# Kernel tuning notes

Hardware: AMD Instinct MI355X
Metric: run time of the kernel (lower is better)

## Reference

```python
import jax, jax.numpy as jnp
import numpy as np

EPS = 1e-5
B, N, NPOINT, K = 16, 4096, 1024, 32
IN_CH, OUT_CH = 64, 64


def index_points(points, idx):
    # points: [B, N, C], idx: [B, ...] -> [B, ..., C]
    b = points.shape[0]
    flat = idx.reshape(b, -1)
    out = jnp.take_along_axis(points, flat[:, :, None], axis=1)
    return out.reshape(idx.shape + (points.shape[-1],))


def bn2d(x, gamma, beta):
    # x: [B, C, H, W], batch-stat BN (training mode), biased variance
    m = x.mean(axis=(0, 2, 3), keepdims=True)
    v = x.var(axis=(0, 2, 3), keepdims=True)
    return gamma[None, :, None, None] * (x - m) / jnp.sqrt(v + EPS) + beta[None, :, None, None]


def bn1d(x, gamma, beta):
    # x: [B, C, L]
    m = x.mean(axis=(0, 2), keepdims=True)
    v = x.var(axis=(0, 2), keepdims=True)
    return gamma[None, :, None] * (x - m) / jnp.sqrt(v + EPS) + beta[None, :, None]


def conv1x1(x, w, b):
    # x: [B, C, H, W], w: [O, C], b: [O]
    return jnp.einsum('bchw,oc->bohw', x, w) + b[None, :, None, None]


def setup_inputs() -> dict:
    key = jax.random.key(0)
    ks = jax.random.split(key, 16)
    inp = {
        'xyz': jax.random.normal(ks[0], (B, N, 3), jnp.float32),
        'points': jax.random.normal(ks[1], (B, N, 61), jnp.float32),
        'local_coordinates': jax.random.normal(ks[2], (B, NPOINT * K, 3), jnp.float32),
        'neighbor_lists': jax.random.randint(ks[3], (B, NPOINT, K), 0, N),
        'data_idx': jax.random.randint(ks[4], (B, NPOINT), 0, N),
        # WeightNet: 3 -> 16 -> 16 -> OUT_CH, each conv1x1 + BN2d + relu
        'w0': jax.random.normal(ks[5], (16, 3), jnp.float32) * 0.1,
        'b0': jnp.zeros((16,), jnp.float32),
        'g0': jnp.ones((16,), jnp.float32),
        'be0': jnp.zeros((16,), jnp.float32),
        'w1': jax.random.normal(ks[6], (16, 16), jnp.float32) * 0.1,
        'b1': jnp.zeros((16,), jnp.float32),
        'g1': jnp.ones((16,), jnp.float32),
        'be1': jnp.zeros((16,), jnp.float32),
        'w2': jax.random.normal(ks[7], (OUT_CH, 16), jnp.float32) * 0.1,
        'b2': jnp.zeros((OUT_CH,), jnp.float32),
        'g2': jnp.ones((OUT_CH,), jnp.float32),
        'be2': jnp.zeros((OUT_CH,), jnp.float32),
        # bn_conv over IN_CH*OUT_CH channels
        'gc': jnp.ones((IN_CH * OUT_CH,), jnp.float32),
        'bc': jnp.zeros((IN_CH * OUT_CH,), jnp.float32),
        # linear IN_CH*OUT_CH -> OUT_CH
        'lw': jax.random.normal(ks[8], (IN_CH * OUT_CH, OUT_CH), jnp.float32) * 0.01,
        'lb': jnp.zeros((OUT_CH,), jnp.float32),
        # bn_linear
        'gl': jnp.ones((OUT_CH,), jnp.float32),
        'bl': jnp.zeros((OUT_CH,), jnp.float32),
    }
    return inp


def reference(xyz, points, local_coordinates, neighbor_lists, data_idx,
              w0, b0, g0, be0, w1, b1, g1, be1, w2, b2, g2, be2,
              gc, bc, lw, lb, gl, bl):
    new_xyz = index_points(xyz, data_idx)                       # [B, NPOINT, 3]
    pts = jnp.concatenate([points, xyz], axis=2)                # [B, N, IN_CH]
    grouped = index_points(pts, neighbor_lists)                 # [B, NPOINT, K, IN_CH]
    grouped = grouped.transpose(0, 1, 3, 2)                     # [B, NPOINT, IN_CH, K]

    # WeightNet on local coordinates
    lc = local_coordinates.reshape(B, NPOINT, K, 3).transpose(0, 3, 2, 1)  # [B, 3, K, NPOINT]
    h = jax.nn.relu(bn2d(conv1x1(lc, w0, b0), g0, be0))
    h = jax.nn.relu(bn2d(conv1x1(h, w1, b1), g1, be1))
    h = jax.nn.relu(bn2d(conv1x1(h, w2, b2), g2, be2))          # [B, OUT_CH, K, NPOINT]
    weights = h.transpose(0, 3, 2, 1)                            # [B, NPOINT, K, OUT_CH]

    # aggregate over neighbors: [B, NPOINT, IN_CH, OUT_CH]
    new_points = jnp.einsum('bnik,bnko->bnio', grouped, weights)
    new_points = new_points.reshape(B, NPOINT, IN_CH * OUT_CH)

    new_points = jax.nn.relu(
        bn1d(new_points.transpose(0, 2, 1), gc, bc).transpose(0, 2, 1))
    new_points = new_points @ lw + lb                            # [B, NPOINT, OUT_CH]
    new_points = bn1d(new_points.transpose(0, 2, 1), gl, bl).transpose(0, 2, 1)
    new_points = jax.nn.relu(new_points)
    return (new_xyz, new_points)
```

## Files before the change

kernel.cpp:

```cpp
#include <hip/hip_runtime.h>
#include <hip/hip_bf16.h>

#define BB 16
#define NN 4096
#define NPOINTS 1024
#define KK 32
#define NPTS (BB*NPOINTS)
#define NWN  (BB*NPOINTS*KK)
#define EPSF 1e-5f
#define SGBLK 512
#define SGIT  4

typedef unsigned short u16;
typedef u16  u16x8 __attribute__((ext_vector_type(8)));
typedef u16  u16x4 __attribute__((ext_vector_type(4)));
typedef short s16x8 __attribute__((ext_vector_type(8)));
typedef float f32x4 __attribute__((ext_vector_type(4)));
typedef float f32x4u __attribute__((ext_vector_type(4), aligned(4)));

__device__ __forceinline__ float bf(u16 u){
  union { unsigned int i; float f; } v; v.i = ((unsigned int)u) << 16; return v.f;
}
__device__ __forceinline__ u16 f2b(float f){
  __hip_bfloat16 h = __float2bfloat16(f);
  union { __hip_bfloat16 hh; u16 u; } v; v.hh = h; return v.u;
}


__global__ __launch_bounds__(256) void k_init(const float* xyz, const int* didx, float* out,
                                              const float* lw, u16* lwbt,
                                              const float* points, u16* ptsw,
                                              const float* lc, float* PA){
  int t = threadIdx.x;
  if (blockIdx.x < 64){
    int p = blockIdx.x * 256 + t;
    int b = p >> 10;
    int idx = didx[p];
    const float* src = xyz + ((size_t)(b * NN + idx)) * 3;
    float* dst = out + (size_t)p * 3;
    dst[0] = src[0]; dst[1] = src[1]; dst[2] = src[2];
  } else if (blockIdx.x < 128){
    __shared__ float T[64][65];
    int ib = blockIdx.x - 64;
    int kb = ib * 64;
    {
      int k = t >> 2, c4 = t & 3;
      #pragma unroll
      for (int j = 0; j < 4; ++j)
        *(f32x4*)&T[k][c4*16 + j*4] = *(const f32x4*)(lw + (size_t)(kb + k)*64 + c4*16 + j*4);
    }
    __syncthreads();
    {
      int n = t >> 2, k4 = t & 3;
      #pragma unroll
      for (int j = 0; j < 16; ++j){
        int k = k4*16 + j;
        lwbt[(size_t)n*4096 + k*64 + ib] = f2b(T[k][n]);
      }
    }
  } else if (blockIdx.x < 640){
    int gid0 = (blockIdx.x - 128) * 256 + t;
    #pragma unroll
    for (int rep = 0; rep < 4; ++rep){
      int idx = gid0 + rep * 131072;
      int row = idx >> 3, c8 = idx & 7;
      const float* prow = points + (size_t)row * 61;
      u16x8 g;
      if (c8 < 7){
        f32x4 lo = *(const f32x4u*)(prow + c8*8);
        f32x4 hi = *(const f32x4u*)(prow + c8*8 + 4);
        g[0]=f2b(lo.x); g[1]=f2b(lo.y); g[2]=f2b(lo.z); g[3]=f2b(lo.w);
        g[4]=f2b(hi.x); g[5]=f2b(hi.y); g[6]=f2b(hi.z); g[7]=f2b(hi.w);
      } else {
        const float* xr = xyz + (size_t)row * 3;
        f32x4 lo = *(const f32x4u*)(prow + 56);
        g[0]=f2b(lo.x); g[1]=f2b(lo.y); g[2]=f2b(lo.z); g[3]=f2b(lo.w);
        g[4]=f2b(prow[60]);
        g[5]=f2b(xr[0]); g[6]=f2b(xr[1]); g[7]=f2b(xr[2]);
      }
      *(u16x8*)(ptsw + (size_t)row*64 + c8*8) = g;
    }
  } else {
    int bid = blockIdx.x - 640;
    float a[9];
    #pragma unroll
    for (int r = 0; r < 9; ++r) a[r] = 0.f;
    size_t base = (size_t)bid * 1024 + t;
    for (int ip = 0; ip < 4; ++ip){
      size_t p = base + (size_t)ip * 256;
      float x0 = lc[p*3], x1 = lc[p*3+1], x2 = lc[p*3+2];
      a[0]+=x0; a[1]+=x1; a[2]+=x2;
      a[3]+=x0*x0; a[4]+=x0*x1; a[5]+=x0*x2;
      a[6]+=x1*x1; a[7]+=x1*x2; a[8]+=x2*x2;
    }
    #pragma unroll
    for (int m = 1; m < 64; m <<= 1){
      #pragma unroll
      for (int r = 0; r < 9; ++r) a[r] += __shfl_xor(a[r], m);
    }
    if ((t & 63) == 0){
      float* dst = PA + (size_t)(bid*4 + (t>>6)) * 16;
      f32x4 v0 = {a[0],a[1],a[2],a[3]}, v1 = {a[4],a[5],a[6],a[7]}, v2 = {a[8],0.f,0.f,0.f};
      *(f32x4*)dst = v0; *(f32x4*)(dst+4) = v1; *(f32x4*)(dst+8) = v2;
    }
  }
}

__global__ __launch_bounds__(256) void k_red0(const float* PA, const float* w0, const float* b0,
                                              const float* g0, const float* be0, float* F){
  __shared__ float ms[12];
  __shared__ float a0sh[16];
  int t = threadIdx.x;
  if (t < 12){
    float s0=0,s1=0,s2=0,s3=0;
    const float* p = PA + t;
    for (int r = 0; r < 2048; r += 4){
      s0 += p[(size_t)(r+0)*16]; s1 += p[(size_t)(r+1)*16];
      s2 += p[(size_t)(r+2)*16]; s3 += p[(size_t)(r+3)*16];
    }
    ms[t] = (s0+s1)+(s2+s3);
  }
  __syncthreads();
  if (t < 16){
    float wx = w0[t*3], wy = w0[t*3+1], wz = w0[t*3+2], bb = b0[t];
    float lin = wx*ms[0] + wy*ms[1] + wz*ms[2];
    float quad = wx*wx*ms[3] + wy*wy*ms[6] + wz*wz*ms[8]
               + 2.f*(wx*wy*ms[4] + wx*wz*ms[5] + wy*wz*ms[7]);
    float S = lin + (float)NWN * bb;
    float Q = quad + 2.f*bb*lin + (float)NWN*bb*bb;
    float m = S * (1.f/NWN);
    float v = Q * (1.f/NWN) - m*m;
    float a = g0[t] * rsqrtf(v + EPSF);
    float d = be0[t] - m*a;
    a0sh[t] = a;
    F[48+t] = a*bb + d;
  }
  __syncthreads();
  if (t < 48) F[t] = a0sh[t/3] * w0[t];
}

__global__ __launch_bounds__(256) void k_statG1(const float* lc, const float* F, float* PB){
  __shared__ f32x4 w0p[16];
  __shared__ __align__(16) u16 Ht[4][16*72];
  __shared__ float GS[4][16][17];
  __shared__ float SHs[4][16];
  int t = threadIdx.x;
  int w = t >> 6, l = t & 63;
  if (t < 16){
    f32x4 wv = {F[t*3], F[t*3+1], F[t*3+2], F[48+t]};
    w0p[t] = wv;
  }
  __syncthreads();
  f32x4 acc = {0.f,0.f,0.f,0.f};
  float sh[16];
  #pragma unroll
  for (int r = 0; r < 16; ++r) sh[r] = 0.f;
  u16* Hw = &Ht[w][0];
  for (int it = 0; it < SGIT; ++it){
    size_t p = (size_t)blockIdx.x * (SGIT*256) + (size_t)it*256 + w*64 + l;
    float x0 = lc[p*3], x1 = lc[p*3+1], x2 = lc[p*3+2];
    float h[16];
    #pragma unroll
    for (int oc = 0; oc < 16; ++oc){
      f32x4 wv = w0p[oc];
      h[oc] = fmaxf(0.f, wv.x*x0 + wv.y*x1 + wv.z*x2 + wv.w);
      sh[oc] += h[oc];
    }
    #pragma unroll
    for (int c = 0; c < 16; ++c) Hw[c*72 + l] = f2b(h[c]);
    __syncthreads();
    #pragma unroll
    for (int tt = 0; tt < 2; ++tt){
      s16x8 af = *(const s16x8*)&Hw[(l & 15)*72 + tt*32 + (l >> 4)*8];
      acc = __builtin_amdgcn_mfma_f32_16x16x32_bf16(af, af, acc, 0, 0, 0);
    }
    __syncthreads();
  }
  #pragma unroll
  for (int r = 0; r < 4; ++r)
    GS[w][(l>>4)*4 + r][l & 15] = acc[r];
  #pragma unroll
  for (int m = 1; m < 64; m <<= 1){
    #pragma unroll
    for (int r = 0; r < 16; ++r) sh[r] += __shfl_xor(sh[r], m);
  }
  if (l == 0){
    #pragma unroll
    for (int r = 0; r < 16; ++r) SHs[w][r] = sh[r];
  }
  __syncthreads();
  {
    int i = t >> 4, j = t & 15;
    float g = GS[0][i][j] + GS[1][i][j] + GS[2][i][j] + GS[3][i][j];
    PB[(size_t)blockIdx.x*272 + t] = g;
    if (t < 16)
      PB[(size_t)blockIdx.x*272 + 256 + t] = SHs[0][t]+SHs[1][t]+SHs[2][t]+SHs[3][t];
  }
}

__global__ __launch_bounds__(256) void k_statG2(const float* lc, const float* F,
                                                const u16* w1Bg, float* PB){
  __shared__ f32x4 w0p[16];
  __shared__ __align__(16) u16 Ht0[4][64*40];
  __shared__ __align__(16) u16 Ht1[4][16*72];
  __shared__ float GS[4][16][17];
  __shared__ float SHs[4][16];
  int t = threadIdx.x;
  int w = t >> 6, l = t & 63;
  if (t < 16){
    f32x4 wv = {F[t*3], F[t*3+1], F[t*3+2], F[48+t]};
    w0p[t] = wv;
  }
  s16x8 w1B = *(const s16x8*)&w1Bg[l*8];
  float b1f = F[320 + (l & 15)];
  u16* H0w = &Ht0[w][0];
  u16* H1w = &Ht1[w][0];
  {
    u16x8 z8 = {0,0,0,0,0,0,0,0};
    *(u16x8*)&H0w[l*40 + 16] = z8;
    *(u16x8*)&H0w[l*40 + 24] = z8;
  }
  __syncthreads();
  f32x4 acc = {0.f,0.f,0.f,0.f};
  float shloc = 0.f;
  for (int it = 0; it < SGIT; ++it){
    size_t p = (size_t)blockIdx.x * (SGIT*256) + (size_t)it*256 + w*64 + l;
    float x0 = lc[p*3], x1 = lc[p*3+1], x2 = lc[p*3+2];
    u16x8 p0, p1;
    #pragma unroll
    for (int oc = 0; oc < 8; ++oc){
      f32x4 wv = w0p[oc];
      p0[oc] = f2b(fmaxf(0.f, wv.x*x0 + wv.y*x1 + wv.z*x2 + wv.w));
    }
    #pragma unroll
    for (int oc = 0; oc < 8; ++oc){
      f32x4 wv = w0p[8+oc];
      p1[oc] = f2b(fmaxf(0.f, wv.x*x0 + wv.y*x1 + wv.z*x2 + wv.w));
    }
    *(u16x8*)&H0w[l*40]     = p0;
    *(u16x8*)&H0w[l*40 + 8] = p1;
    __syncthreads();
    #pragma unroll
    for (int mt = 0; mt < 4; ++mt){
      s16x8 af = *(const s16x8*)&H0w[(mt*16 + (l & 15))*40 + (l >> 4)*8];
      f32x4 c = {b1f, b1f, b1f, b1f};
      c = __builtin_amdgcn_mfma_f32_16x16x32_bf16(af, w1B, c, 0, 0, 0);
      #pragma unroll
      for (int r = 0; r < 4; ++r){
        float v = fmaxf(0.f, c[r]);
        shloc += v;
        H1w[(l & 15)*72 + mt*16 + (l >> 4)*4 + r] = f2b(v);
      }
    }
    __syncthreads();
    #pragma unroll
    for (int tt = 0; tt < 2; ++tt){
      s16x8 afg = *(const s16x8*)&H1w[(l & 15)*72 + tt*32 + (l >> 4)*8];
      acc = __builtin_amdgcn_mfma_f32_16x16x32_bf16(afg, afg, acc, 0, 0, 0);
    }
    __syncthreads();
  }
  #pragma unroll
  for (int r = 0; r < 4; ++r)
    GS[w][(l>>4)*4 + r][l & 15] = acc[r];
  shloc += __shfl_xor(shloc, 16);
  shloc += __shfl_xor(shloc, 32);
  if (l < 16) SHs[w][l] = shloc;
  __syncthreads();
  {
    int i = t >> 4, j = t & 15;
    float g = GS[0][i][j] + GS[1][i][j] + GS[2][i][j] + GS[3][i][j];
    PB[(size_t)blockIdx.x*272 + t] = g;
    if (t < 16)
      PB[(size_t)blockIdx.x*272 + 256 + t] = SHs[0][t]+SHs[1][t]+SHs[2][t]+SHs[3][t];
  }
}

__global__ __launch_bounds__(256) void k_red1(const float* PB, const float* w1, const float* b1,
                                              const float* g1, const float* be1, float* F,
                                              u16* w1Bg){
  __shared__ float red[272];
  __shared__ float a1sh[16];
  int t = threadIdx.x;
  for (int e = t; e < 272; e += 256){
    float s = 0.f;
    for (int r = 0; r < SGBLK; ++r) s += PB[(size_t)r*272 + e];
    red[e] = s;
  }
  __syncthreads();
  if (t < 16){
    float wv[16];
    #pragma unroll
    for (int ic = 0; ic < 16; ++ic) wv[ic] = w1[t*16+ic];
    float lin = 0.f;
    #pragma unroll
    for (int ic = 0; ic < 16; ++ic) lin += wv[ic]*red[256+ic];
    float quad = 0.f;
    for (int i = 0; i < 16; ++i){
      float ri = 0.f;
      #pragma unroll
      for (int j = 0; j < 16; ++j) ri += wv[j]*red[i*16+j];
      quad += wv[i]*ri;
    }
    float bb = b1[t];
    float S = lin + (float)NWN * bb;
    float Q = quad + 2.f*bb*lin + (float)NWN*bb*bb;
    float m = S * (1.f/NWN);
    float v = Q * (1.f/NWN) - m*m;
    float a = g1[t] * rsqrtf(v + EPSF);
    float d = be1[t] - m*a;
    a1sh[t] = a;
    F[320+t] = a*bb + d;
  }
  __syncthreads();
  F[64 + t] = a1sh[t >> 4] * w1[t];
  if (t < 64){
    int oc = t & 15, icb = (t >> 4) * 8;
    u16x8 fr;
    #pragma unroll
    for (int j = 0; j < 8; ++j){
      int ic = icb + j;
      fr[j] = (ic < 16) ? f2b(a1sh[oc] * w1[oc*16 + ic]) : (u16)0;
    }
    *(u16x8*)&w1Bg[t*8] = fr;
  }
}

__global__ __launch_bounds__(256) void k_red2(const float* PB, const float* w2, const float* b2,
                                              const float* g2, const float* be2, float* F,
                                              u16* w2Bg){
  __shared__ float red[272];
  __shared__ float a2sh[64];
  int t = threadIdx.x;
  for (int e = t; e < 272; e += 256){
    float s = 0.f;
    for (int r = 0; r < SGBLK; ++r) s += PB[(size_t)r*272 + e];
    red[e] = s;
  }
  __syncthreads();
  if (t < 64){
    float wv[16];
    #pragma unroll
    for (int ic = 0; ic < 16; ++ic) wv[ic] = w2[t*16+ic];
    float lin = 0.f;
    #pragma unroll
    for (int ic = 0; ic < 16; ++ic) lin += wv[ic]*red[256+ic];
    float quad = 0.f;
    for (int i = 0; i < 16; ++i){
      float ri = 0.f;
      #pragma unroll
      for (int j = 0; j < 16; ++j) ri += wv[j]*red[i*16+j];
      quad += wv[i]*ri;
    }
    float bb = b2[t];
    float S = lin + (float)NWN * bb;
    float Q = quad + 2.f*bb*lin + (float)NWN*bb*bb;
    float m = S * (1.f/NWN);
    float v = Q * (1.f/NWN) - m*m;
    float a = g2[t] * rsqrtf(v + EPSF);
    float d = be2[t] - m*a;
    a2sh[t] = a;
    F[1360+t] = a*bb + d;
  }
  __syncthreads();
  for (int i = t; i < 1024; i += 256) F[336+i] = a2sh[i >> 4] * w2[i];
  {
    int ot = t >> 6, lane = t & 63;
    int oc = ot*16 + (lane & 15), icb = ((lane >> 4)) * 8;
    u16x8 fr;
    #pragma unroll
    for (int j = 0; j < 8; ++j){
      int ic = icb + j;
      fr[j] = (ic < 16) ? f2b(a2sh[oc] * w2[oc*16 + ic]) : (u16)0;
    }
    *(u16x8*)&w2Bg[t*8] = fr;
  }
}

__global__ __launch_bounds__(256) void k_main(const float* lcg, const int* nbrg,
    const u16* ptsw, const float* F,
    const u16* w1Bg, const u16* w2Bg,
    u16* npw){
  __shared__ __align__(16) u16 Gr[2][64*40];
  __shared__ __align__(16) u16 WrBuf[2][64*40];
  __shared__ __align__(16) u16 H1bf[2][32*40];
  int t = threadIdx.x;
  int w = t >> 6, l = t & 63;
  int p0 = blockIdx.x * 2;
  s16x8 w1B  = *(const s16x8*)&w1Bg[l*8];
  s16x8 w2B0 = *(const s16x8*)&w2Bg[(0*64 + l)*8];
  s16x8 w2B1 = *(const s16x8*)&w2Bg[(1*64 + l)*8];
  s16x8 w2B2 = *(const s16x8*)&w2Bg[(2*64 + l)*8];
  s16x8 w2B3 = *(const s16x8*)&w2Bg[(3*64 + l)*8];
  float b1f  = F[320 + (l & 15)];
  float b2f0 = F[1360 +  0 + (l & 15)];
  float b2f1 = F[1360 + 16 + (l & 15)];
  float b2f2 = F[1360 + 32 + (l & 15)];
  float b2f3 = F[1360 + 48 + (l & 15)];
  int oc0 = (t & 7) * 2;
  f32x4 w0a = {F[oc0*3], F[oc0*3+1], F[oc0*3+2], F[48+oc0]};
  f32x4 w0b = {F[oc0*3+3], F[oc0*3+4], F[oc0*3+5], F[48+oc0+1]};
  {
    int k = t >> 3, c = 16 + (t & 7)*2;
    *(unsigned int*)&WrBuf[0][k*40 + c] = 0u;
    *(unsigned int*)&WrBuf[1][k*40 + c] = 0u;
    *(unsigned int*)&H1bf[0][k*40 + c] = 0u;
    *(unsigned int*)&H1bf[1][k*40 + c] = 0u;
  }
  {
    int kg = w*8 + (l >> 3), c8 = l & 7;
    int kphys = ((w ^ (c8 & 3)) << 3) + (l >> 3);
    #pragma unroll
    for (int pt = 0; pt < 2; ++pt){
      int point = p0 + pt;
      int bbp = point >> 10;
      int n = nbrg[(size_t)point*32 + kg];
      u16x8 g = *(const u16x8*)(ptsw + (size_t)(bbp * NN + n)*64 + c8*8);
      #pragma unroll
      for (int j = 0; j < 8; ++j)
        Gr[pt][(c8*8 + j)*40 + kphys] = g[j];
    }
  }
  {
    int k = t >> 3;
    #pragma unroll
    for (int pt = 0; pt < 2; ++pt){
      const float* xp = lcg + (size_t)(p0 + pt)*96 + k*3;
      float x0 = xp[0], x1 = xp[1], x2 = xp[2];
      WrBuf[pt][k*40 + oc0]     = f2b(fmaxf(0.f, w0a.x*x0 + w0a.y*x1 + w0a.z*x2 + w0a.w));
      WrBuf[pt][k*40 + oc0 + 1] = f2b(fmaxf(0.f, w0b.x*x0 + w0b.y*x1 + w0b.z*x2 + w0b.w));
    }
  }
  __syncthreads();
  {
    int pt = w >> 1, kt = w & 1;
    s16x8 af = *(const s16x8*)&WrBuf[pt][(kt*16 + (l & 15))*40 + (l >> 4)*8];
    f32x4 acc = {b1f, b1f, b1f, b1f};
    acc = __builtin_amdgcn_mfma_f32_16x16x32_bf16(af, w1B, acc, 0, 0, 0);
    #pragma unroll
    for (int r = 0; r < 4; ++r)
      H1bf[pt][(kt*16 + (l >> 4)*4 + r)*40 + (l & 15)] = f2b(fmaxf(0.f, acc[r]));
  }
  __syncthreads();
  {
    int pt = w & 1, kt = w >> 1;
    s16x8 af = *(const s16x8*)&H1bf[pt][(kt*16 + (l & 15))*40 + (l >> 4)*8];
    int kbase = kt*16 + (l >> 4)*4;
    f32x4 a0c = {b2f0,b2f0,b2f0,b2f0};
    a0c = __builtin_amdgcn_mfma_f32_16x16x32_bf16(af, w2B0, a0c, 0, 0, 0);
    u16x4 s0v; s0v[0]=f2b(fmaxf(0.f,a0c[0])); s0v[1]=f2b(fmaxf(0.f,a0c[1]));
    s0v[2]=f2b(fmaxf(0.f,a0c[2])); s0v[3]=f2b(fmaxf(0.f,a0c[3]));
    *(u16x4*)&WrBuf[pt][( 0 + (l & 15))*40 + kbase] = s0v;
    f32x4 a1c = {b2f1,b2f1,b2f1,b2f1};
    a1c = __builtin_amdgcn_mfma_f32_16x16x32_bf16(af, w2B1, a1c, 0, 0, 0);
    u16x4 s1v; s1v[0]=f2b(fmaxf(0.f,a1c[0])); s1v[1]=f2b(fmaxf(0.f,a1c[1]));
    s1v[2]=f2b(fmaxf(0.f,a1c[2])); s1v[3]=f2b(fmaxf(0.f,a1c[3]));
    *(u16x4*)&WrBuf[pt][(16 + (l & 15))*40 + kbase] = s1v;
    f32x4 a2c = {b2f2,b2f2,b2f2,b2f2};
    a2c = __builtin_amdgcn_mfma_f32_16x16x32_bf16(af, w2B2, a2c, 0, 0, 0);
    u16x4 s2v; s2v[0]=f2b(fmaxf(0.f,a2c[0])); s2v[1]=f2b(fmaxf(0.f,a2c[1]));
    s2v[2]=f2b(fmaxf(0.f,a2c[2])); s2v[3]=f2b(fmaxf(0.f,a2c[3]));
    *(u16x4*)&WrBuf[pt][(32 + (l & 15))*40 + kbase] = s2v;
    f32x4 a3c = {b2f3,b2f3,b2f3,b2f3};
    a3c = __builtin_amdgcn_mfma_f32_16x16x32_bf16(af, w2B3, a3c, 0, 0, 0);
    u16x4 s3v; s3v[0]=f2b(fmaxf(0.f,a3c[0])); s3v[1]=f2b(fmaxf(0.f,a3c[1]));
    s3v[2]=f2b(fmaxf(0.f,a3c[2])); s3v[3]=f2b(fmaxf(0.f,a3c[3]));
    *(u16x4*)&WrBuf[pt][(48 + (l & 15))*40 + kbase] = s3v;
  }
  __syncthreads();
  {
    int li = l & 15, lkb = l >> 4, lr = (l >> 4) * 4;
    #pragma unroll
    for (int pt = 0; pt < 2; ++pt){
      s16x8 bfrag = *(const s16x8*)&WrBuf[pt][(w*16 + li)*40 + lkb*8];
      size_t obase = (size_t)(p0 + pt)*4096 + (size_t)(w*16 + li)*64 + lr;
      #pragma unroll
      for (int it = 0; it < 4; ++it){
        int ch = it*16 + li;
        int key = (ch >> 3) & 3;
        s16x8 afrag = *(const s16x8*)&Gr[pt][ch*40 + ((lkb ^ key) << 3)];
        f32x4 z = {0.f, 0.f, 0.f, 0.f};
        f32x4 d = __builtin_amdgcn_mfma_f32_16x16x32_bf16(afrag, bfrag, z, 0, 0, 0);
        u16x4 st;
        st[0] = f2b(d[0]); st[1] = f2b(d[1]); st[2] = f2b(d[2]); st[3] = f2b(d[3]);
        *(u16x4*)(npw + obase + it*16) = st;
      }
    }
  }
}

__global__ __launch_bounds__(256) void k_statC(const u16* npw, float* PC){
  int t = threadIdx.x;
  float s[16], q[16];
  #pragma unroll
  for (int j = 0; j < 16; ++j){ s[j] = 0.f; q[j] = 0.f; }
  size_t rowbase = (size_t)blockIdx.x * 64;
  for (int p = 0; p < 64; ++p){
    const u16* row = npw + (rowbase + p) * 4096 + t * 16;
    u16x8 a = *(const u16x8*)row;
    u16x8 b = *(const u16x8*)(row + 8);
    #pragma unroll
    for (int j = 0; j < 8; ++j){ float v = bf(a[j]); s[j]   += v; q[j]   += v*v; }
    #pragma unroll
    for (int j = 0; j < 8; ++j){ float v = bf(b[j]); s[8+j] += v; q[8+j] += v*v; }
  }
  float* dst = PC + (size_t)blockIdx.x * 8192 + t * 16;
  #pragma unroll
  for (int j = 0; j < 16; ++j){ dst[j] = s[j]; dst[4096 + j] = q[j]; }
}

__global__ __launch_bounds__(256) void k_finC(const float* PC, const float* gc, const float* bc,
                                              float* AC, float* DC){
  int qpos = blockIdx.x * 256 + threadIdx.x;
  float s = 0.f, q = 0.f;
  for (int r = 0; r < 256; ++r){
    s += PC[(size_t)r * 8192 + qpos];
    q += PC[(size_t)r * 8192 + 4096 + qpos];
  }
  int ch = (qpos & 63)*64 + (qpos >> 6);
  float m = s * (1.f/16384.f);
  float v = q * (1.f/16384.f) - m*m;
  float a = gc[ch] * rsqrtf(v + EPSF);
  AC[qpos] = a; DC[qpos] = bc[ch] - m*a;
}

__global__ __launch_bounds__(256) void k_linear(const u16* npw, const float* AC, const float* DC,
                                                const u16* lwbt, const float* lb, float* yw,
                                                float* PL){
  __shared__ u16 Al[2][16*72];
  __shared__ u16 Bl[2][64*72];
  __shared__ float cps[64], cpq[64];
  int t = threadIdx.x;
  int w = t >> 6, l = t & 63;
  int rowbase = blockIdx.x * 16;
  int rA = t >> 4, cA = t & 15;
  int nB = t >> 3, cB = t & 7;
  const u16* Aptr  = npw  + (size_t)(rowbase + rA)*4096 + cA*4;
  const u16* B0ptr = lwbt + (size_t)nB*4096 + cB*8;
  const u16* B1ptr = lwbt + (size_t)(nB + 32)*4096 + cB*8;
  f32x4 acc0 = {0.f,0.f,0.f,0.f};
  u16x4 uA  = *(const u16x4*)(Aptr);
  u16x8 uB0 = *(const u16x8*)(B0ptr);
  u16x8 uB1 = *(const u16x8*)(B1ptr);
  {
    int kk = cA*4;
    f32x4 av = *(const f32x4*)(AC + kk);
    f32x4 dv = *(const f32x4*)(DC + kk);
    u16x4 o;
    o[0] = f2b(fmaxf(0.f, av.x*bf(uA[0]) + dv.x));
    o[1] = f2b(fmaxf(0.f, av.y*bf(uA[1]) + dv.y));
    o[2] = f2b(fmaxf(0.f, av.z*bf(uA[2]) + dv.z));
    o[3] = f2b(fmaxf(0.f, av.w*bf(uA[3]) + dv.w));
    *(u16x4*)&Al[0][rA*72 + cA*4] = o;
    *(u16x8*)&Bl[0][nB*72 + cB*8]        = uB0;
    *(u16x8*)&Bl[0][(nB + 32)*72 + cB*8] = uB1;
  }
  uA  = *(const u16x4*)(Aptr + 64);
  uB0 = *(const u16x8*)(B0ptr + 64);
  uB1 = *(const u16x8*)(B1ptr + 64);
  __syncthreads();
  int cur = 0;
  for (int kb = 0; kb < 4096; kb += 64){
    if (kb + 64 < 4096){
      int kk = kb + 64 + cA*4;
      f32x4 av = *(const f32x4*)(AC + kk);
      f32x4 dv = *(const f32x4*)(DC + kk);
      u16x4 o;
      o[0] = f2b(fmaxf(0.f, av.x*bf(uA[0]) + dv.x));
      o[1] = f2b(fmaxf(0.f, av.y*bf(uA[1]) + dv.y));
      o[2] = f2b(fmaxf(0.f, av.z*bf(uA[2]) + dv.z));
      o[3] = f2b(fmaxf(0.f, av.w*bf(uA[3]) + dv.w));
      *(u16x4*)&Al[cur^1][rA*72 + cA*4] = o;
      *(u16x8*)&Bl[cur^1][nB*72 + cB*8]        = uB0;
      *(u16x8*)&Bl[cur^1][(nB + 32)*72 + cB*8] = uB1;
      if (kb + 128 < 4096){
        uA  = *(const u16x4*)(Aptr + kb + 128);
        uB0 = *(const u16x8*)(B0ptr + kb + 128);
        uB1 = *(const u16x8*)(B1ptr + kb + 128);
      }
    }
    #pragma unroll
    for (int ks = 0; ks < 2; ++ks){
      s16x8 af  = *(const s16x8*)&Al[cur][((l & 15))*72 + ks*32 + (l >> 4)*8];
      s16x8 bf0 = *(const s16x8*)&Bl[cur][(w*16 + (l & 15))*72 + ks*32 + (l >> 4)*8];
      acc0 = __builtin_amdgcn_mfma_f32_16x16x32_bf16(af, bf0, acc0, 0, 0, 0);
    }
    __syncthreads();
    cur ^= 1;
  }
  int col0 = w*16 + (l & 15);
  float lb0 = lb[col0];
  float s0 = 0.f, q0 = 0.f;
  if (t < 64){ cps[t] = 0.f; cpq[t] = 0.f; }
  __syncthreads();
  #pragma unroll
  for (int r = 0; r < 4; ++r){
    int row = rowbase + (l >> 4)*4 + r;
    float y0 = acc0[r] + lb0;
    yw[(size_t)row*64 + col0] = y0;
    s0 += y0; q0 += y0*y0;
  }
  atomicAdd(&cps[col0], s0); atomicAdd(&cpq[col0], q0);
  __syncthreads();
  if (t < 64){
    PL[blockIdx.x*128 + t]      = cps[t];
    PL[blockIdx.x*128 + 64 + t] = cpq[t];
  }
}

__global__ __launch_bounds__(128) void k_redF(const float* PL, float* SL){
  int t = threadIdx.x;
  float s = 0.f;
  for (int b = 0; b < 1024; ++b) s += PL[b*128 + t];
  SL[t] = s;
}

__global__ __launch_bounds__(256) void k_final(const float* yw, const float* SL,
                                               const float* gl, const float* bl, float* out){
  int e = (blockIdx.x * 256 + threadIdx.x) * 4;
  int o = e & 63;
  f32x4 y = *(const f32x4*)(yw + e);
  f32x4 r;
  #pragma unroll
  for (int j = 0; j < 4; ++j){
    float m = SL[o+j] * (1.f/16384.f);
    float v = SL[64+o+j] * (1.f/16384.f) - m*m;
    float a = gl[o+j] * rsqrtf(v + EPSF);
    float d = bl[o+j] - m*a;
    r[j] = fmaxf(0.f, a*y[j] + d);
  }
  *(f32x4*)(out + 49152 + e) = r;
}

extern "C" void kernel_launch(void* const* d_in, const int* in_sizes, int n_in,
                              void* d_out, int out_size, void* d_ws, size_t ws_size,
                              hipStream_t stream){
  (void)in_sizes; (void)n_in; (void)out_size; (void)ws_size;
  const float* xyz    = (const float*)d_in[0];
  const float* points = (const float*)d_in[1];
  const float* lc     = (const float*)d_in[2];
  const int*   nbrl   = (const int*)d_in[3];
  const int*   didx   = (const int*)d_in[4];
  const float* w0 = (const float*)d_in[5];
  const float* b0 = (const float*)d_in[6];
  const float* g0 = (const float*)d_in[7];
  const float* be0= (const float*)d_in[8];
  const float* w1 = (const float*)d_in[9];
  const float* b1 = (const float*)d_in[10];
  const float* g1 = (const float*)d_in[11];
  const float* be1= (const float*)d_in[12];
  const float* w2 = (const float*)d_in[13];
  const float* b2 = (const float*)d_in[14];
  const float* g2 = (const float*)d_in[15];
  const float* be2= (const float*)d_in[16];
  const float* gc = (const float*)d_in[17];
  const float* bc = (const float*)d_in[18];
  const float* lw = (const float*)d_in[19];
  const float* lb = (const float*)d_in[20];
  const float* gl = (const float*)d_in[21];
  const float* bl = (const float*)d_in[22];
  float* out = (float*)d_out;
  char* ws = (char*)d_ws;

  float* F   = (float*)ws;
  float* SL  = F + 1536;
  float* AC  = SL + 128;
  float* DC  = AC + 4096;
  float* PA  = DC + 4096;
  float* PB1 = PA + 32768;
  float* PB2 = PB1 + 139264;
  float* PL  = PB2 + 139264;
  u16*  w1Bg = (u16*)(PL + 131072);
  u16*  w2Bg = w1Bg + 512;
  float* PC  = (float*)(ws + 4194304);
  u16*  npw  = (u16*)(ws + 4194304 + 8388608);
  float* yw  = (float*)(ws + 4194304 + 8388608 + 134217728);
  u16*  lwbt = (u16*)(ws + 4194304 + 8388608 + 134217728 + 4194304);
  u16*  ptsw = (u16*)(ws + 4194304 + 8388608 + 134217728 + 4194304 + 1048576);

  k_init  <<<1152,  256, 0, stream>>>(xyz, didx, out, lw, lwbt, points, ptsw, lc, PA);
  k_red0  <<<1,     256, 0, stream>>>(PA, w0, b0, g0, be0, F);
  k_statG1<<<SGBLK, 256, 0, stream>>>(lc, F, PB1);
  k_red1  <<<1,     256, 0, stream>>>(PB1, w1, b1, g1, be1, F, w1Bg);
  k_statG2<<<SGBLK, 256, 0, stream>>>(lc, F, w1Bg, PB2);
  k_red2  <<<1,     256, 0, stream>>>(PB2, w2, b2, g2, be2, F, w2Bg);
  k_main  <<<8192,  256, 0, stream>>>(lc, nbrl, ptsw, F, w1Bg, w2Bg, npw);
  k_statC <<<256,   256, 0, stream>>>(npw, PC);
  k_finC  <<<16,    256, 0, stream>>>(PC, gc, bc, AC, DC);
  k_linear<<<1024,  256, 0, stream>>>(npw, AC, DC, lwbt, lb, yw, PL);
  k_redF  <<<1,     128, 0, stream>>>(PL, SL);
  k_final <<<1024,  256, 0, stream>>>(yw, SL, gl, bl, out);
}
```

Before: 257.9 us.

## Fuse BN-conv statistics into main kernel and loop over point groups per block

The main aggregation kernel now handles 16 points per block in a loop and accumulates per-channel sum and sum-of-squares in registers from the fp32 MFMA outputs. It writes per-block partials directly, which removes the separate statC pass that re-read the large bf16 intermediate. The finC reduction is split across more blocks with a shared-memory tree to reduce serial latency. The workspace layout is rearranged so yw aliases PC. Statistics now come from fp32 values instead of the bf16-rounded ones, and having fewer blocks lowers parallelism in the main kernel.

```diff
diff --git a/kernel.cpp b/kernel.cpp
--- a/kernel.cpp
+++ b/kernel.cpp
@@ -380,13 +380,13 @@
 __global__ __launch_bounds__(256) void k_main(const float* lcg, const int* nbrg,
     const u16* ptsw, const float* F,
     const u16* w1Bg, const u16* w2Bg,
-    u16* npw){
+    u16* npw, float* PC){
   __shared__ __align__(16) u16 Gr[2][64*40];
   __shared__ __align__(16) u16 WrBuf[2][64*40];
   __shared__ __align__(16) u16 H1bf[2][32*40];
   int t = threadIdx.x;
   int w = t >> 6, l = t & 63;
-  int p0 = blockIdx.x * 2;
+  int pbase = blockIdx.x * 16;
   s16x8 w1B  = *(const s16x8*)&w1Bg[l*8];
   s16x8 w2B0 = *(const s16x8*)&w2Bg[(0*64 + l)*8];
   s16x8 w2B1 = *(const s16x8*)&w2Bg[(1*64 + l)*8];
@@ -402,126 +402,143 @@
   f32x4 w0b = {F[oc0*3+3], F[oc0*3+4], F[oc0*3+5], F[48+oc0+1]};
   {
     int k = t >> 3, c = 16 + (t & 7)*2;
-    *(unsigned int*)&WrBuf[0][k*40 + c] = 0u;
-    *(unsigned int*)&WrBuf[1][k*40 + c] = 0u;
     *(unsigned int*)&H1bf[0][k*40 + c] = 0u;
     *(unsigned int*)&H1bf[1][k*40 + c] = 0u;
   }
+  float sacc[16], qacc[16];
+  #pragma unroll
+  for (int j = 0; j < 16; ++j){ sacc[j] = 0.f; qacc[j] = 0.f; }
+  __syncthreads();
+
+  for (int g = 0; g < 8; ++g){
+    int p0 = pbase + g*2;
+    {
+      int kg = w*8 + (l >> 3), c8 = l & 7;
+      int kphys = ((w ^ (c8 & 3)) << 3) + (l >> 3);
+      #pragma unroll
+      for (int pt = 0; pt < 2; ++pt){
+        int point = p0 + pt;
+        int bbp = point >> 10;
+        int n = nbrg[(size_t)point*32 + kg];
+        u16x8 gv = *(const u16x8*)(ptsw + (size_t)(bbp * NN + n)*64 + c8*8);
+        #pragma unroll
+        for (int j = 0; j < 8; ++j)
+          Gr[pt][(c8*8 + j)*40 + kphys] = gv[j];
+      }
+    }
+    {
+      int k = t >> 3, cpad = 16 + (t & 7)*2;
+      #pragma unroll
+      for (int pt = 0; pt < 2; ++pt){
+        const float* xp = lcg + (size_t)(p0 + pt)*96 + k*3;
+        float x0 = xp[0], x1 = xp[1], x2 = xp[2];
+        WrBuf[pt][k*40 + oc0]     = f2b(fmaxf(0.f, w0a.x*x0 + w0a.y*x1 + w0a.z*x2 + w0a.w));
+        WrBuf[pt][k*40 + oc0 + 1] = f2b(fmaxf(0.f, w0b.x*x0 + w0b.y*x1 + w0b.z*x2 + w0b.w));
+        *(unsigned int*)&WrBuf[pt][k*40 + cpad] = 0u;
+      }
+    }
+    __syncthreads();
+    {
+      int pt = w >> 1, kt = w & 1;
+      s16x8 af = *(const s16x8*)&WrBuf[pt][(kt*16 + (l & 15))*40 + (l >> 4)*8];
+      f32x4 acc = {b1f, b1f, b1f, b1f};
+      acc = __builtin_amdgcn_mfma_f32_16x16x32_bf16(af, w1B, acc, 0, 0, 0);
+      #pragma unroll
+      for (int r = 0; r < 4; ++r)
+        H1bf[pt][(kt*16 + (l >> 4)*4 + r)*40 + (l & 15)] = f2b(fmaxf(0.f, acc[r]));
+    }
+    __syncthreads();
+    {
+      int pt = w & 1, kt = w >> 1;
+      s16x8 af = *(const s16x8*)&H1bf[pt][(kt*16 + (l & 15))*40 + (l >> 4)*8];
+      int kbase = kt*16 + (l >> 4)*4;
+      f32x4 a0c = {b2f0,b2f0,b2f0,b2f0};
+      a0c = __builtin_amdgcn_mfma_f32_16x16x32_bf16(af, w2B0, a0c, 0, 0, 0);
+      u16x4 s0v; s0v[0]=f2b(fmaxf(0.f,a0c[0])); s0v[1]=f2b(fmaxf(0.f,a0c[1]));
+      s0v[2]=f2b(fmaxf(0.f,a0c[2])); s0v[3]=f2b(fmaxf(0.f,a0c[3]));
+      *(u16x4*)&WrBuf[pt][( 0 + (l & 15))*40 + kbase] = s0v;
+      f32x4 a1c = {b2f1,b2f1,b2f1,b2f1};
+      a1c = __builtin_amdgcn_mfma_f32_16x16x32_bf16(af, w2B1, a1c, 0, 0, 0);
+      u16x4 s1v; s1v[0]=f2b(fmaxf(0.f,a1c[0])); s1v[1]=f2b(fmaxf(0.f,a1c[1]));
+      s1v[2]=f2b(fmaxf(0.f,a1c[2])); s1v[3]=f2b(fmaxf(0.f,a1c[3]));
+      *(u16x4*)&WrBuf[pt][(16 + (l & 15))*40 + kbase] = s1v;
+      f32x4 a2c = {b2f2,b2f2,b2f2,b2f2};
+      a2c = __builtin_amdgcn_mfma_f32_16x16x32_bf16(af, w2B2, a2c, 0, 0, 0);
+      u16x4 s2v; s2v[0]=f2b(fmaxf(0.f,a2c[0])); s2v[1]=f2b(fmaxf(0.f,a2c[1]));
+      s2v[2]=f2b(fmaxf(0.f,a2c[2])); s2v[3]=f2b(fmaxf(0.f,a2c[3]));
+      *(u16x4*)&WrBuf[pt][(32 + (l & 15))*40 + kbase] = s2v;
+      f32x4 a3c = {b2f3,b2f3,b2f3,b2f3};
+      a3c = __builtin_amdgcn_mfma_f32_16x16x32_bf16(af, w2B3, a3c, 0, 0, 0);
+      u16x4 s3v; s3v[0]=f2b(fmaxf(0.f,a3c[0])); s3v[1]=f2b(fmaxf(0.f,a3c[1]));
+      s3v[2]=f2b(fmaxf(0.f,a3c[2])); s3v[3]=f2b(fmaxf(0.f,a3c[3]));
+      *(u16x4*)&WrBuf[pt][(48 + (l & 15))*40 + kbase] = s3v;
+    }
+    __syncthreads();
+    {
+      int li = l & 15, lkb = l >> 4, lr = (l >> 4) * 4;
+      #pragma unroll
+      for (int pt = 0; pt < 2; ++pt){
+        s16x8 bfrag = *(const s16x8*)&WrBuf[pt][(w*16 + li)*40 + lkb*8];
+        size_t obase = (size_t)(p0 + pt)*4096 + (size_t)(w*16 + li)*64 + lr;
+        #pragma unroll
+        for (int it = 0; it < 4; ++it){
+          int ch = it*16 + li;
+          int key = (ch >> 3) & 3;
+          s16x8 afrag = *(const s16x8*)&Gr[pt][ch*40 + ((lkb ^ key) << 3)];
+          f32x4 z = {0.f, 0.f, 0.f, 0.f};
+          f32x4 d = __builtin_amdgcn_mfma_f32_16x16x32_bf16(afrag, bfrag, z, 0, 0, 0);
+          u16x4 st;
+          st[0] = f2b(d[0]); st[1] = f2b(d[1]); st[2] = f2b(d[2]); st[3] = f2b(d[3]);
+          *(u16x4*)(npw + obase + it*16) = st;
+          #pragma unroll
+          for (int r = 0; r < 4; ++r){
+            sacc[it*4 + r] += d[r];
+            qacc[it*4 + r] += d[r]*d[r];
+          }
+        }
+      }
+    }
+    __syncthreads();
+  }
   {
-    int kg = w*8 + (l >> 3), c8 = l & 7;
-    int kphys = ((w ^ (c8 & 3)) << 3) + (l >> 3);
-    #pragma unroll
-    for (int pt = 0; pt < 2; ++pt){
-      int point = p0 + pt;
-      int bbp = point >> 10;
-      int n = nbrg[(size_t)point*32 + kg];
-      u16x8 g = *(const u16x8*)(ptsw + (size_t)(bbp * NN + n)*64 + c8*8);
-      #pragma unroll
-      for (int j = 0; j < 8; ++j)
-        Gr[pt][(c8*8 + j)*40 + kphys] = g[j];
-    }
-  }
-  {
-    int k = t >> 3;
-    #pragma unroll
-    for (int pt = 0; pt < 2; ++pt){
-      const float* xp = lcg + (size_t)(p0 + pt)*96 + k*3;
-      float x0 = xp[0], x1 = xp[1], x2 = xp[2];
-      WrBuf[pt][k*40 + oc0]     = f2b(fmaxf(0.f, w0a.x*x0 + w0a.y*x1 + w0a.z*x2 + w0a.w));
-      WrBuf[pt][k*40 + oc0 + 1] = f2b(fmaxf(0.f, w0b.x*x0 + w0b.y*x1 + w0b.z*x2 + w0b.w));
-    }
-  }
-  __syncthreads();
-  {
-    int pt = w >> 1, kt = w & 1;
-    s16x8 af = *(const s16x8*)&WrBuf[pt][(kt*16 + (l & 15))*40 + (l >> 4)*8];
-    f32x4 acc = {b1f, b1f, b1f, b1f};
-    acc = __builtin_amdgcn_mfma_f32_16x16x32_bf16(af, w1B, acc, 0, 0, 0);
-    #pragma unroll
-    for (int r = 0; r < 4; ++r)
-      H1bf[pt][(kt*16 + (l >> 4)*4 + r)*40 + (l & 15)] = f2b(fmaxf(0.f, acc[r]));
-  }
-  __syncthreads();
-  {
-    int pt = w & 1, kt = w >> 1;
-    s16x8 af = *(const s16x8*)&H1bf[pt][(kt*16 + (l & 15))*40 + (l >> 4)*8];
-    int kbase = kt*16 + (l >> 4)*4;
-    f32x4 a0c = {b2f0,b2f0,b2f0,b2f0};
-    a0c = __builtin_amdgcn_mfma_f32_16x16x32_bf16(af, w2B0, a0c, 0, 0, 0);
-    u16x4 s0v; s0v[0]=f2b(fmaxf(0.f,a0c[0])); s0v[1]=f2b(fmaxf(0.f,a0c[1]));
-    s0v[2]=f2b(fmaxf(0.f,a0c[2])); s0v[3]=f2b(fmaxf(0.f,a0c[3]));
-    *(u16x4*)&WrBuf[pt][( 0 + (l & 15))*40 + kbase] = s0v;
-    f32x4 a1c = {b2f1,b2f1,b2f1,b2f1};
-    a1c = __builtin_amdgcn_mfma_f32_16x16x32_bf16(af, w2B1, a1c, 0, 0, 0);
-    u16x4 s1v; s1v[0]=f2b(fmaxf(0.f,a1c[0])); s1v[1]=f2b(fmaxf(0.f,a1c[1]));
-    s1v[2]=f2b(fmaxf(0.f,a1c[2])); s1v[3]=f2b(fmaxf(0.f,a1c[3]));
-    *(u16x4*)&WrBuf[pt][(16 + (l & 15))*40 + kbase] = s1v;
-    f32x4 a2c = {b2f2,b2f2,b2f2,b2f2};
-    a2c = __builtin_amdgcn_mfma_f32_16x16x32_bf16(af, w2B2, a2c, 0, 0, 0);
-    u16x4 s2v; s2v[0]=f2b(fmaxf(0.f,a2c[0])); s2v[1]=f2b(fmaxf(0.f,a2c[1]));
-    s2v[2]=f2b(fmaxf(0.f,a2c[2])); s2v[3]=f2b(fmaxf(0.f,a2c[3]));
-    *(u16x4*)&WrBuf[pt][(32 + (l & 15))*40 + kbase] = s2v;
-    f32x4 a3c = {b2f3,b2f3,b2f3,b2f3};
-    a3c = __builtin_amdgcn_mfma_f32_16x16x32_bf16(af, w2B3, a3c, 0, 0, 0);
-    u16x4 s3v; s3v[0]=f2b(fmaxf(0.f,a3c[0])); s3v[1]=f2b(fmaxf(0.f,a3c[1]));
-    s3v[2]=f2b(fmaxf(0.f,a3c[2])); s3v[3]=f2b(fmaxf(0.f,a3c[3]));
-    *(u16x4*)&WrBuf[pt][(48 + (l & 15))*40 + kbase] = s3v;
-  }
-  __syncthreads();
-  {
-    int li = l & 15, lkb = l >> 4, lr = (l >> 4) * 4;
-    #pragma unroll
-    for (int pt = 0; pt < 2; ++pt){
-      s16x8 bfrag = *(const s16x8*)&WrBuf[pt][(w*16 + li)*40 + lkb*8];
-      size_t obase = (size_t)(p0 + pt)*4096 + (size_t)(w*16 + li)*64 + lr;
-      #pragma unroll
-      for (int it = 0; it < 4; ++it){
-        int ch = it*16 + li;
-        int key = (ch >> 3) & 3;
-        s16x8 afrag = *(const s16x8*)&Gr[pt][ch*40 + ((lkb ^ key) << 3)];
-        f32x4 z = {0.f, 0.f, 0.f, 0.f};
-        f32x4 d = __builtin_amdgcn_mfma_f32_16x16x32_bf16(afrag, bfrag, z, 0, 0, 0);
-        u16x4 st;
-        st[0] = f2b(d[0]); st[1] = f2b(d[1]); st[2] = f2b(d[2]); st[3] = f2b(d[3]);
-        *(u16x4*)(npw + obase + it*16) = st;
-      }
-    }
-  }
-}
-
-__global__ __launch_bounds__(256) void k_statC(const u16* npw, float* PC){
-  int t = threadIdx.x;
-  float s[16], q[16];
-  #pragma unroll
-  for (int j = 0; j < 16; ++j){ s[j] = 0.f; q[j] = 0.f; }
-  size_t rowbase = (size_t)blockIdx.x * 64;
-  for (int p = 0; p < 64; ++p){
-    const u16* row = npw + (rowbase + p) * 4096 + t * 16;
-    u16x8 a = *(const u16x8*)row;
-    u16x8 b = *(const u16x8*)(row + 8);
-    #pragma unroll
-    for (int j = 0; j < 8; ++j){ float v = bf(a[j]); s[j]   += v; q[j]   += v*v; }
-    #pragma unroll
-    for (int j = 0; j < 8; ++j){ float v = bf(b[j]); s[8+j] += v; q[8+j] += v*v; }
-  }
-  float* dst = PC + (size_t)blockIdx.x * 8192 + t * 16;
-  #pragma unroll
-  for (int j = 0; j < 16; ++j){ dst[j] = s[j]; dst[4096 + j] = q[j]; }
+    int qb = (w*16 + (l & 15))*64 + (l >> 4)*4;
+    float* dst = PC + (size_t)blockIdx.x * 8192;
+    #pragma unroll
+    for (int it = 0; it < 4; ++it){
+      f32x4 sv = {sacc[it*4+0], sacc[it*4+1], sacc[it*4+2], sacc[it*4+3]};
+      f32x4 qv = {qacc[it*4+0], qacc[it*4+1], qacc[it*4+2], qacc[it*4+3]};
+      *(f32x4*)(dst + qb + it*16) = sv;
+      *(f32x4*)(dst + 4096 + qb + it*16) = qv;
+    }
+  }
 }
 
 __global__ __launch_bounds__(256) void k_finC(const float* PC, const float* gc, const float* bc,
                                               float* AC, float* DC){
-  int qpos = blockIdx.x * 256 + threadIdx.x;
+  __shared__ float shs[16][17], shq[16][17];
+  int t = threadIdx.x;
+  int ql = t & 15, rc = t >> 4;
+  int qpos = blockIdx.x * 16 + ql;
   float s = 0.f, q = 0.f;
-  for (int r = 0; r < 256; ++r){
+  int r0 = rc * 64;
+  #pragma unroll 4
+  for (int r = r0; r < r0 + 64; ++r){
     s += PC[(size_t)r * 8192 + qpos];
     q += PC[(size_t)r * 8192 + 4096 + qpos];
   }
-  int ch = (qpos & 63)*64 + (qpos >> 6);
-  float m = s * (1.f/16384.f);
-  float v = q * (1.f/16384.f) - m*m;
-  float a = gc[ch] * rsqrtf(v + EPSF);
-  AC[qpos] = a; DC[qpos] = bc[ch] - m*a;
+  shs[ql][rc] = s; shq[ql][rc] = q;
+  __syncthreads();
+  if (t < 16){
+    float ss = 0.f, qq = 0.f;
+    #pragma unroll
+    for (int c = 0; c < 16; ++c){ ss += shs[t][c]; qq += shq[t][c]; }
+    int qp = blockIdx.x * 16 + t;
+    int ch = (qp & 63)*64 + (qp >> 6);
+    float m = ss * (1.f/16384.f);
+    float v = qq * (1.f/16384.f) - m*m;
+    float a = gc[ch] * rsqrtf(v + EPSF);
+    AC[qp] = a; DC[qp] = bc[ch] - m*a;
+  }
 }
 
 __global__ __launch_bounds__(256) void k_linear(const u16* npw, const float* AC, const float* DC,
@@ -672,11 +689,11 @@
   float* PL  = PB2 + 139264;
   u16*  w1Bg = (u16*)(PL + 131072);
   u16*  w2Bg = w1Bg + 512;
+  u16*  lwbt = (u16*)(ws + 2097152);
   float* PC  = (float*)(ws + 4194304);
-  u16*  npw  = (u16*)(ws + 4194304 + 8388608);
-  float* yw  = (float*)(ws + 4194304 + 8388608 + 134217728);
-  u16*  lwbt = (u16*)(ws + 4194304 + 8388608 + 134217728 + 4194304);
-  u16*  ptsw = (u16*)(ws + 4194304 + 8388608 + 134217728 + 4194304 + 1048576);
+  float* yw  = (float*)(ws + 4194304);
+  u16*  npw  = (u16*)(ws + 37748736);
+  u16*  ptsw = (u16*)(ws + 171966464);
 
   k_init  <<<1152,  256, 0, stream>>>(xyz, didx, out, lw, lwbt, points, ptsw, lc, PA);
   k_red0  <<<1,     256, 0, stream>>>(PA, w0, b0, g0, be0, F);
@@ -684,9 +701,8 @@
   k_red1  <<<1,     256, 0, stream>>>(PB1, w1, b1, g1, be1, F, w1Bg);
   k_statG2<<<SGBLK, 256, 0, stream>>>(lc, F, w1Bg, PB2);
   k_red2  <<<1,     256, 0, stream>>>(PB2, w2, b2, g2, be2, F, w2Bg);
-  k_main  <<<8192,  256, 0, stream>>>(lc, nbrl, ptsw, F, w1Bg, w2Bg, npw);
-  k_statC <<<256,   256, 0, stream>>>(npw, PC);
-  k_finC  <<<16,    256, 0, stream>>>(PC, gc, bc, AC, DC);
+  k_main  <<<1024,  256, 0, stream>>>(lc, nbrl, ptsw, F, w1Bg, w2Bg, npw, PC);
+  k_finC  <<<256,   256, 0, stream>>>(PC, gc, bc, AC, DC);
   k_linear<<<1024,  256, 0, stream>>>(npw, AC, DC, lwbt, lb, yw, PL);
   k_redF  <<<1,     128, 0, stream>>>(PL, SL);
   k_final <<<1024,  256, 0, stream>>>(yw, SL, gl, bl, out);
```

Result: faster. 249.3 us (-3.3%).
